# Optimization experiments

Hardware: AMD Instinct MI355X
Metric: run time of the kernel (lower is better)

## Reference

```python
import math
import jax, jax.numpy as jnp
import numpy as np

B, T, HID, H, D = 2, 2048, 1024, 16, 64
EPS = 1e-5


def score_norm(s):
    # standardize scores over the key axis (per row), as in RealFormer-style score normalization
    mu = jnp.mean(s, axis=-1, keepdims=True)
    sd = jnp.std(s, axis=-1, keepdims=True)
    return (s - mu) / (sd + EPS)


def setup_inputs() -> dict:
    key = jax.random.key(0)
    ks = jax.random.split(key, 9)
    w_scale = 1.0 / math.sqrt(HID)
    return {
        "x": jax.random.normal(ks[0], (B, T, HID), dtype=jnp.float32),
        "s_prev": jax.random.normal(ks[1], (B, H, T, T), dtype=jnp.float32),
        "Wq": jax.random.normal(ks[2], (HID, H * D), dtype=jnp.float32) * w_scale,
        "Wk": jax.random.normal(ks[3], (HID, H * D), dtype=jnp.float32) * w_scale,
        "Wv": jax.random.normal(ks[4], (HID, H * D), dtype=jnp.float32) * w_scale,
        "Wo": jax.random.normal(ks[5], (H * D, HID), dtype=jnp.float32) * w_scale,
        "alpha": jnp.zeros((H,), dtype=jnp.float32),   # alpha_init = 0.0
        "gamma": jnp.ones((H,), dtype=jnp.float32),    # gamma_init = 1.0
        "beta": jnp.zeros((H,), dtype=jnp.float32),    # beta_init = 0.0
    }


def reference(x, s_prev, Wq, Wk, Wv, Wo, alpha, gamma, beta):
    Bx, t, _ = x.shape
    # project and split heads: [B, H, t, D]
    def split(h):
        return h.reshape(Bx, t, H, D).transpose(0, 2, 1, 3)
    Q = split(x @ Wq)
    K = split(x @ Wk)
    V = split(x @ Wv)

    raw = jnp.einsum('bhtd,bhsd->bhts', Q, K) / math.sqrt(D)

    # gated residual score term (s_prev detached: residual_grad_flow=False)
    gate = jax.nn.sigmoid(alpha)[None, :, None, None]
    scale = gamma[None, :, None, None]
    shift = beta[None, :, None, None]
    r = gate * (scale * score_norm(jax.lax.stop_gradient(s_prev)) + shift)
    raw = raw + r

    # causal mask (t > 1 path)
    causal = jnp.triu(jnp.ones((t, t), dtype=bool), k=1)  # True above diagonal
    scores = jnp.where(causal[None, None], -jnp.inf, raw)

    w = jax.nn.softmax(scores, axis=-1)
    ctx = jnp.einsum('bhts,bhsd->bhtd', w, V)
    merged = ctx.transpose(0, 2, 1, 3).reshape(Bx, t, H * D)
    out = merged @ Wo
    return out, raw
```

## Files before the change

kernel.cpp:

```cpp
#include <hip/hip_runtime.h>

typedef __attribute__((ext_vector_type(4))) float f32x4;
typedef __attribute__((ext_vector_type(8))) short s16x8;
typedef __attribute__((ext_vector_type(4))) unsigned short u16x4;
typedef unsigned short ushortT;

__device__ inline ushortT f2bf(float f) {
  union { float f; unsigned u; } v; v.f = f;
  unsigned r = v.u + 0x7fffu + ((v.u >> 16) & 1u);
  return (ushortT)(r >> 16);
}
__device__ inline float bf2f(ushortT s) {
  union { unsigned u; float f; } v; v.u = ((unsigned)s) << 16;
  return v.f;
}
__device__ inline unsigned pk_bf16(float lo, float hi) {
  unsigned r;
  asm("v_cvt_pk_bf16_f32 %0, %1, %2" : "=v"(r) : "v"(lo), "v"(hi));
  return r;
}
__device__ inline ushortT cvt1_bf16(float f) {
  unsigned r;
  asm("v_cvt_pk_bf16_f32 %0, %1, %2" : "=v"(r) : "v"(f), "v"(f));
  return (ushortT)r;
}
__device__ inline f32x4 mfma16(s16x8 a, s16x8 b, f32x4 c) {
  return __builtin_amdgcn_mfma_f32_16x16x32_bf16(a, b, c, 0, 0, 0);
}
typedef const __attribute__((address_space(1))) unsigned GU;
typedef __attribute__((address_space(3))) unsigned LU;
__device__ inline void gload_lds16(const void* g, void* l) {
  __builtin_amdgcn_global_load_lds((GU*)g, (LU*)l, 16, 0, 0);
}

#define BARRIER_LIGHT() do {                                  \
    __builtin_amdgcn_sched_barrier(0);                        \
    asm volatile("s_waitcnt lgkmcnt(0)" ::: "memory");        \
    __builtin_amdgcn_s_barrier();                             \
    __builtin_amdgcn_sched_barrier(0);                        \
  } while (0)

__global__ void conv_bf16(const float* __restrict__ in, ushortT* __restrict__ o) {
  size_t i = ((size_t)blockIdx.x * 256 + threadIdx.x) * 4;
  f32x4 v = *(const f32x4*)(in + i);
  u16x4 u = { f2bf(v[0]), f2bf(v[1]), f2bf(v[2]), f2bf(v[3]) };
  *(u16x4*)(o + i) = u;
}

__global__ void transp_bf16(const float* __restrict__ Wm, ushortT* __restrict__ wt) {
  __shared__ float t[32][33];
  int bx = blockIdx.x, by = blockIdx.y;
  int x = threadIdx.x, y = threadIdx.y;
#pragma unroll
  for (int i = 0; i < 32; i += 8)
    t[y + i][x] = Wm[(size_t)(by * 32 + y + i) * 1024 + bx * 32 + x];
  __syncthreads();
#pragma unroll
  for (int i = 0; i < 32; i += 8)
    wt[(size_t)(bx * 32 + y + i) * 1024 + by * 32 + x] = f2bf(t[x][y + i]);
}

template <int MODE>
__global__ __launch_bounds__(256) void gemm_bt(const ushortT* __restrict__ A,
                                               const ushortT* __restrict__ Bt,
                                               ushortT* __restrict__ o0,
                                               ushortT* __restrict__ o1,
                                               ushortT* __restrict__ o2,
                                               float* __restrict__ of) {
  __shared__ ushortT lA[128 * 32];
  __shared__ ushortT lB[128 * 32];
  const int tid = threadIdx.x;
  const int w = tid >> 6, l = tid & 63;
  const int a = l & 15, hi = l >> 4;
  const int wr = w >> 1, wc = w & 1;
  const int row0 = blockIdx.y * 128, col0 = blockIdx.x * 128;
  f32x4 acc[4][4] = {};
  const int r1 = tid >> 2, c1 = tid & 3;
  const int r2 = (tid + 256) >> 2, c2 = (tid + 256) & 3;
  for (int k0 = 0; k0 < 1024; k0 += 32) {
    __syncthreads();
    gload_lds16(A + (size_t)(row0 + r1) * 1024 + k0 + c1 * 8, &lA[r1 * 32 + c1 * 8]);
    gload_lds16(A + (size_t)(row0 + r2) * 1024 + k0 + c2 * 8, &lA[r2 * 32 + c2 * 8]);
    gload_lds16(Bt + (size_t)(col0 + r1) * 1024 + k0 + c1 * 8, &lB[r1 * 32 + c1 * 8]);
    gload_lds16(Bt + (size_t)(col0 + r2) * 1024 + k0 + c2 * 8, &lB[r2 * 32 + c2 * 8]);
    __syncthreads();
    s16x8 af[4], bfr[4];
#pragma unroll
    for (int m = 0; m < 4; ++m)
      af[m] = *(const s16x8*)&lA[(wr * 64 + m * 16 + a) * 32 + hi * 8];
#pragma unroll
    for (int n = 0; n < 4; ++n)
      bfr[n] = *(const s16x8*)&lB[(wc * 64 + n * 16 + a) * 32 + hi * 8];
#pragma unroll
    for (int m = 0; m < 4; ++m)
#pragma unroll
      for (int n = 0; n < 4; ++n)
        acc[m][n] = mfma16(af[m], bfr[n], acc[m][n]);
  }
  const int proj = col0 >> 10;
#pragma unroll
  for (int m = 0; m < 4; ++m)
#pragma unroll
    for (int n = 0; n < 4; ++n) {
      const int gr0 = row0 + wr * 64 + m * 16 + hi * 4;
      const int gc = col0 + wc * 64 + n * 16 + a;
#pragma unroll
      for (int r = 0; r < 4; ++r) {
        const int gr = gr0 + r;
        float v = acc[m][n][r];
        if (MODE == 0) {
          const int bb = gr >> 11, t = gr & 2047;
          const int cc = gc & 1023;
          const int hh = cc >> 6, d = cc & 63;
          const size_t bh = (size_t)bb * 16 + hh;
          if (proj == 0)      o0[(bh * 2048 + t) * 64 + d] = f2bf(v * 0.125f);
          else if (proj == 1) o1[(bh * 2048 + t) * 64 + d] = f2bf(v);
          else                o2[(bh * 64 + d) * 2048 + t] = f2bf(v);
        } else {
          of[(size_t)gr * 1024 + gc] = v;
        }
      }
    }
}

#define SBS 2056
__global__ __launch_bounds__(512, 4) void attn_fused(
    const ushortT* __restrict__ qw, const ushortT* __restrict__ kw,
    const ushortT* __restrict__ vtw, const float* __restrict__ sprev,
    const float* __restrict__ alpha, const float* __restrict__ gamma,
    const float* __restrict__ beta, float* __restrict__ raw,
    ushortT* __restrict__ merged) {
  __shared__ ushortT sb[16 * SBS];
  __shared__ float c0_s[16], c1_s[16], li_s[16];
  __shared__ float red[4][64][4];
  const int j = blockIdx.x;
  const int h = blockIdx.y, b = blockIdx.z;
  const int bh = b * 16 + h;
  const int tid = threadIdx.x;
  const int w = tid >> 6, l = tid & 63;
  const int a = l & 15, hi = l >> 4;

  const float gate = 1.f / (1.f + __expf(-alpha[h]));
  const float gm = gamma[h], bt = beta[h];
  const ushortT* kb = kw + (size_t)bh * 2048 * 64;
  const float* spb = sprev + (size_t)bh * 2048 * 2048;

  f32x4 pre[2][8];
  {
    const int t0 = j * 16;
#pragma unroll
    for (int rr = 0; rr < 2; ++rr) {
      const float* rp = spb + (size_t)(t0 + 2 * w + rr) * 2048 + 4 * l;
#pragma unroll
      for (int i = 0; i < 8; ++i) pre[rr][i] = *(const f32x4*)(rp + 256 * i);
    }
  }

  for (int it = 0; it < 4; ++it) {
    const int t0 = j * 16 + it * 512;
    BARRIER_LIGHT();

#pragma unroll
    for (int rr = 0; rr < 2; ++rr) {
      const int row = 2 * w + rr;
      float sum = 0.f, sq = 0.f;
#pragma unroll
      for (int i = 0; i < 8; ++i) {
        f32x4 v = pre[rr][i];
        sum += v[0] + v[1] + v[2] + v[3];
        sq += v[0] * v[0] + v[1] * v[1] + v[2] * v[2] + v[3] * v[3];
        uint2 u;
        u.x = pk_bf16(v[0], v[1]);
        u.y = pk_bf16(v[2], v[3]);
        *(uint2*)&sb[row * SBS + 4 * l + 256 * i] = u;
      }
#pragma unroll
      for (int s = 32; s >= 1; s >>= 1) {
        sum += __shfl_xor(sum, s);
        sq += __shfl_xor(sq, s);
      }
      if (l == 0) {
        float mu = sum * (1.f / 2048.f);
        float var = fmaxf(sq * (1.f / 2048.f) - mu * mu, 0.f);
        float rs = 1.f / (sqrtf(var) + 1e-5f);
        c1_s[row] = gate * gm * rs;
        c0_s[row] = gate * (bt - gm * mu * rs);
      }
    }
    BARRIER_LIGHT();

    const ushortT* qrow = qw + ((size_t)bh * 2048 + t0 + a) * 64;
    s16x8 qf0 = *(const s16x8*)(qrow + hi * 8);
    s16x8 qf1 = *(const s16x8*)(qrow + 32 + hi * 8);
    float c04[4], c14[4];
#pragma unroll
    for (int r = 0; r < 4; ++r) {
      c04[r] = c0_s[4 * hi + r];
      c14[r] = c1_s[4 * hi + r];
    }
    float* rawb = raw + ((size_t)bh * 2048 + t0) * 2048;
    for (int i = 0; i < 16; ++i) {
      const int col0 = (w + 8 * i) * 16;
      const ushortT* kr = kb + (size_t)(col0 + a) * 64 + hi * 8;
      s16x8 kf0 = *(const s16x8*)(kr);
      s16x8 kf1 = *(const s16x8*)(kr + 32);
      f32x4 s4 = {};
      s4 = mfma16(qf0, kf0, s4);
      s4 = mfma16(qf1, kf1, s4);
#pragma unroll
      for (int r = 0; r < 4; ++r) {
        const int rl = 4 * hi + r;
        const float spv = bf2f(sb[rl * SBS + col0 + a]);
        const float rv = fmaf(c14[r], spv, s4[r] + c04[r]);
        rawb[(size_t)rl * 2048 + col0 + a] = rv;
        sb[rl * SBS + col0 + a] = cvt1_bf16((col0 + a) <= (t0 + rl) ? rv : -1e30f);
      }
    }

    if (it < 3) {
      const int t0n = j * 16 + (it + 1) * 512;
#pragma unroll
      for (int rr = 0; rr < 2; ++rr) {
        const float* rp = spb + (size_t)(t0n + 2 * w + rr) * 2048 + 4 * l;
#pragma unroll
        for (int i = 0; i < 8; ++i) pre[rr][i] = *(const f32x4*)(rp + 256 * i);
      }
    }
    BARRIER_LIGHT();

#pragma unroll
    for (int rr = 0; rr < 2; ++rr) {
      const int row = 2 * w + rr;
      float m = -3e38f;
#pragma unroll
      for (int i = 0; i < 16; ++i) {
        unsigned u = *(const unsigned*)&sb[row * SBS + 2 * l + 128 * i];
        union { unsigned u; float f; } lo, hh;
        lo.u = u << 16; hh.u = u & 0xffff0000u;
        m = fmaxf(m, fmaxf(lo.f, hh.f));
      }
#pragma unroll
      for (int s = 32; s >= 1; s >>= 1) m = fmaxf(m, __shfl_xor(m, s));
      float sum = 0.f;
#pragma unroll
      for (int i = 0; i < 16; ++i) {
        unsigned u = *(const unsigned*)&sb[row * SBS + 2 * l + 128 * i];
        union { unsigned u; float f; } lo, hh;
        lo.u = u << 16; hh.u = u & 0xffff0000u;
        float e0 = __expf(lo.f - m);
        float e1 = __expf(hh.f - m);
        sum += e0 + e1;
        *(unsigned*)&sb[row * SBS + 2 * l + 128 * i] = pk_bf16(e0, e1);
      }
#pragma unroll
      for (int s = 32; s >= 1; s >>= 1) sum += __shfl_xor(sum, s);
      if (l == 0) li_s[row] = 1.f / sum;
    }
    BARRIER_LIGHT();

    const int n = w & 3, half = w >> 2;
    const ushortT* vb = vtw + ((size_t)bh * 64 + 16 * n + a) * 2048;
    f32x4 acc = {};
    const int nch = (t0 + 47) >> 5;
    for (int c = half; c < nch; c += 2) {
      s16x8 pf = *(const s16x8*)&sb[a * SBS + 32 * c + 8 * hi];
      s16x8 vf = *(const s16x8*)(vb + 32 * c + 8 * hi);
      acc = mfma16(pf, vf, acc);
    }
    if (half == 1) *(f32x4*)red[n][l] = acc;
    BARRIER_LIGHT();
    if (half == 0) {
      f32x4 o = *(f32x4*)red[n][l];
      acc += o;
#pragma unroll
      for (int r = 0; r < 4; ++r) {
        const int rl = 4 * hi + r;
        const float cx = acc[r] * li_s[rl];
        merged[((size_t)b * 2048 + t0 + rl) * 1024 + h * 64 + 16 * n + a] = f2bf(cx);
      }
    }
  }
}

extern "C" void kernel_launch(void* const* d_in, const int* in_sizes, int n_in,
                              void* d_out, int out_size, void* d_ws, size_t ws_size,
                              hipStream_t stream) {
  (void)in_sizes; (void)n_in; (void)out_size; (void)ws_size;
  const float* x      = (const float*)d_in[0];
  const float* s_prev = (const float*)d_in[1];
  const float* Wq     = (const float*)d_in[2];
  const float* Wk     = (const float*)d_in[3];
  const float* Wv     = (const float*)d_in[4];
  const float* Wo     = (const float*)d_in[5];
  const float* alpha  = (const float*)d_in[6];
  const float* gamma  = (const float*)d_in[7];
  const float* beta   = (const float*)d_in[8];

  float* out = (float*)d_out;
  float* raw = out + (size_t)4194304;

  char* ws = (char*)d_ws;
  const size_t MB = 1024 * 1024;
  ushortT* xb  = (ushortT*)(ws);
  ushortT* wT  = (ushortT*)(ws + 8 * MB);
  ushortT* woT = (ushortT*)(ws + 14 * MB);
  ushortT* qw  = (ushortT*)(ws + 16 * MB);
  ushortT* kw  = (ushortT*)(ws + 24 * MB);
  ushortT* vtw = (ushortT*)(ws + 32 * MB);
  ushortT* mg  = (ushortT*)(ws + 40 * MB);

  conv_bf16<<<4096, 256, 0, stream>>>(x, xb);
  dim3 tb(32, 8);
  transp_bf16<<<dim3(32, 32), tb, 0, stream>>>(Wq, wT);
  transp_bf16<<<dim3(32, 32), tb, 0, stream>>>(Wk, wT + 1024 * 1024);
  transp_bf16<<<dim3(32, 32), tb, 0, stream>>>(Wv, wT + 2 * 1024 * 1024);
  transp_bf16<<<dim3(32, 32), tb, 0, stream>>>(Wo, woT);

  gemm_bt<0><<<dim3(24, 32), 256, 0, stream>>>(xb, wT, qw, kw, vtw, nullptr);

  attn_fused<<<dim3(32, 16, 2), 512, 0, stream>>>(qw, kw, vtw, s_prev, alpha, gamma,
                                                  beta, raw, mg);

  gemm_bt<1><<<dim3(8, 32), 256, 0, stream>>>(mg, woT, nullptr, nullptr, nullptr, out);
}
```

Baseline: 506.3 us.

## Swizzle attention blocks across XCDs, prefetch K/V, use nontemporal s_prev/raw access

The attention launch becomes a 1D grid whose block index is remapped so that consecutive blocks of the same (batch, head) land on the same XCD, which should improve L2 reuse of K and V. s_prev loads and raw stores now use nontemporal hints, since both are streamed once and should not pollute the cache. K fragments are software-prefetched one iteration ahead in the score loop, and the PV loop is unrolled with four V registers loaded ahead. These changes add register pressure, and the swizzle assumes the hardware dispatches blocks round-robin across 8 XCDs.

```diff
diff --git a/kernel.cpp b/kernel.cpp
--- a/kernel.cpp
+++ b/kernel.cpp
@@ -133,8 +133,9 @@
   __shared__ ushortT sb[16 * SBS];
   __shared__ float c0_s[16], c1_s[16], li_s[16];
   __shared__ float red[4][64][4];
-  const int j = blockIdx.x;
-  const int h = blockIdx.y, b = blockIdx.z;
+  const int bid = blockIdx.x;
+  const int wg = (bid & 7) * 128 + (bid >> 3);
+  const int j = wg & 31, h = (wg >> 5) & 15, b = wg >> 9;
   const int bh = b * 16 + h;
   const int tid = threadIdx.x;
   const int w = tid >> 6, l = tid & 63;
@@ -142,7 +143,7 @@
 
   const float gate = 1.f / (1.f + __expf(-alpha[h]));
   const float gm = gamma[h], bt = beta[h];
-  const ushortT* kb = kw + (size_t)bh * 2048 * 64;
+  const ushortT* kbp = kw + (size_t)bh * 2048 * 64;
   const float* spb = sprev + (size_t)bh * 2048 * 2048;
 
   f32x4 pre[2][8];
@@ -152,7 +153,8 @@
     for (int rr = 0; rr < 2; ++rr) {
       const float* rp = spb + (size_t)(t0 + 2 * w + rr) * 2048 + 4 * l;
 #pragma unroll
-      for (int i = 0; i < 8; ++i) pre[rr][i] = *(const f32x4*)(rp + 256 * i);
+      for (int i = 0; i < 8; ++i)
+        pre[rr][i] = __builtin_nontemporal_load((const f32x4*)(rp + 256 * i));
     }
   }
 
@@ -199,22 +201,29 @@
       c14[r] = c1_s[4 * hi + r];
     }
     float* rawb = raw + ((size_t)bh * 2048 + t0) * 2048;
+    const ushortT* kr0 = kbp + (size_t)(w * 16 + a) * 64 + hi * 8;
+    s16x8 ka = *(const s16x8*)(kr0);
+    s16x8 kb2 = *(const s16x8*)(kr0 + 32);
     for (int i = 0; i < 16; ++i) {
       const int col0 = (w + 8 * i) * 16;
-      const ushortT* kr = kb + (size_t)(col0 + a) * 64 + hi * 8;
-      s16x8 kf0 = *(const s16x8*)(kr);
-      s16x8 kf1 = *(const s16x8*)(kr + 32);
+      s16x8 na, nb2;
+      if (i < 15) {
+        const ushortT* krn = kbp + (size_t)(col0 + 128 + a) * 64 + hi * 8;
+        na = *(const s16x8*)(krn);
+        nb2 = *(const s16x8*)(krn + 32);
+      }
       f32x4 s4 = {};
-      s4 = mfma16(qf0, kf0, s4);
-      s4 = mfma16(qf1, kf1, s4);
+      s4 = mfma16(qf0, ka, s4);
+      s4 = mfma16(qf1, kb2, s4);
 #pragma unroll
       for (int r = 0; r < 4; ++r) {
         const int rl = 4 * hi + r;
         const float spv = bf2f(sb[rl * SBS + col0 + a]);
         const float rv = fmaf(c14[r], spv, s4[r] + c04[r]);
-        rawb[(size_t)rl * 2048 + col0 + a] = rv;
+        __builtin_nontemporal_store(rv, &rawb[(size_t)rl * 2048 + col0 + a]);
         sb[rl * SBS + col0 + a] = cvt1_bf16((col0 + a) <= (t0 + rl) ? rv : -1e30f);
       }
+      ka = na; kb2 = nb2;
     }
 
     if (it < 3) {
@@ -223,7 +232,8 @@
       for (int rr = 0; rr < 2; ++rr) {
         const float* rp = spb + (size_t)(t0n + 2 * w + rr) * 2048 + 4 * l;
 #pragma unroll
-        for (int i = 0; i < 8; ++i) pre[rr][i] = *(const f32x4*)(rp + 256 * i);
+        for (int i = 0; i < 8; ++i)
+          pre[rr][i] = __builtin_nontemporal_load((const f32x4*)(rp + 256 * i));
       }
     }
     BARRIER_LIGHT();
@@ -262,10 +272,35 @@
     const ushortT* vb = vtw + ((size_t)bh * 64 + 16 * n + a) * 2048;
     f32x4 acc = {};
     const int nch = (t0 + 47) >> 5;
-    for (int c = half; c < nch; c += 2) {
-      s16x8 pf = *(const s16x8*)&sb[a * SBS + 32 * c + 8 * hi];
-      s16x8 vf = *(const s16x8*)(vb + 32 * c + 8 * hi);
-      acc = mfma16(pf, vf, acc);
+    {
+      s16x8 v0, v1, v2, v3;
+      const int c0i = half;
+      if (c0i + 0 < nch) v0 = *(const s16x8*)(vb + 32 * (c0i + 0) + 8 * hi);
+      if (c0i + 2 < nch) v1 = *(const s16x8*)(vb + 32 * (c0i + 2) + 8 * hi);
+      if (c0i + 4 < nch) v2 = *(const s16x8*)(vb + 32 * (c0i + 4) + 8 * hi);
+      if (c0i + 6 < nch) v3 = *(const s16x8*)(vb + 32 * (c0i + 6) + 8 * hi);
+      for (int cc = c0i; cc < nch; cc += 8) {
+        if (cc + 0 < nch) {
+          s16x8 pf = *(const s16x8*)&sb[a * SBS + 32 * (cc + 0) + 8 * hi];
+          acc = mfma16(pf, v0, acc);
+          if (cc + 8 < nch) v0 = *(const s16x8*)(vb + 32 * (cc + 8) + 8 * hi);
+        }
+        if (cc + 2 < nch) {
+          s16x8 pf = *(const s16x8*)&sb[a * SBS + 32 * (cc + 2) + 8 * hi];
+          acc = mfma16(pf, v1, acc);
+          if (cc + 10 < nch) v1 = *(const s16x8*)(vb + 32 * (cc + 10) + 8 * hi);
+        }
+        if (cc + 4 < nch) {
+          s16x8 pf = *(const s16x8*)&sb[a * SBS + 32 * (cc + 4) + 8 * hi];
+          acc = mfma16(pf, v2, acc);
+          if (cc + 12 < nch) v2 = *(const s16x8*)(vb + 32 * (cc + 12) + 8 * hi);
+        }
+        if (cc + 6 < nch) {
+          s16x8 pf = *(const s16x8*)&sb[a * SBS + 32 * (cc + 6) + 8 * hi];
+          acc = mfma16(pf, v3, acc);
+          if (cc + 14 < nch) v3 = *(const s16x8*)(vb + 32 * (cc + 14) + 8 * hi);
+        }
+      }
     }
     if (half == 1) *(f32x4*)red[n][l] = acc;
     BARRIER_LIGHT();
@@ -318,8 +353,8 @@
 
   gemm_bt<0><<<dim3(24, 32), 256, 0, stream>>>(xb, wT, qw, kw, vtw, nullptr);
 
-  attn_fused<<<dim3(32, 16, 2), 512, 0, stream>>>(qw, kw, vtw, s_prev, alpha, gamma,
-                                                  beta, raw, mg);
+  attn_fused<<<1024, 512, 0, stream>>>(qw, kw, vtw, s_prev, alpha, gamma,
+                                       beta, raw, mg);
 
   gemm_bt<1><<<dim3(8, 32), 256, 0, stream>>>(mg, woT, nullptr, nullptr, nullptr, out);
 }
```

New measurement: 549.6 us. 1.09x slower.
